# Kernel optimization log

Measured on AMD Instinct MI355X. Metric: run time of the kernel, lower is better.

## Reference

```python
import jax, jax.numpy as jnp
import numpy as np

N_NODES = 100000
N_EDGES = 1600000
DIM = 128
N_LAYERS = 3
BN_EPS = 1e-5


def setup_inputs() -> dict:
    key = jax.random.key(0)
    ks = jax.random.split(key, 8)
    x = jax.random.normal(ks[0], (N_NODES, DIM), dtype=jnp.float32)
    edge_index = jax.random.randint(ks[1], (2, N_EDGES), 0, N_NODES, dtype=jnp.int64)
    # Stacked per-layer params (all layers are DIM->DIM since input_dim==hidden_dim)
    W1 = jax.random.normal(ks[2], (N_LAYERS, DIM, DIM), dtype=jnp.float32) * 0.05
    b1 = jnp.zeros((N_LAYERS, DIM), dtype=jnp.float32)
    gamma = jnp.ones((N_LAYERS, DIM), dtype=jnp.float32)
    beta = jnp.zeros((N_LAYERS, DIM), dtype=jnp.float32)
    rmean = jnp.zeros((N_LAYERS, DIM), dtype=jnp.float32)
    rvar = jnp.ones((N_LAYERS, DIM), dtype=jnp.float32)
    W2 = jax.random.normal(ks[3], (N_LAYERS, DIM, DIM), dtype=jnp.float32) * 0.05
    b2 = jnp.zeros((N_LAYERS, DIM), dtype=jnp.float32)
    return {"x": x, "edge_index": edge_index, "W1": W1, "b1": b1,
            "gamma": gamma, "beta": beta, "rmean": rmean, "rvar": rvar,
            "W2": W2, "b2": b2}


def _gin_layer(h, src, dst, W1_l, b1_l, g_l, be_l, m_l, v_l, W2_l, b2_l):
    # adj_t @ h : sum of neighbor (src) features into dst nodes
    agg = jax.ops.segment_sum(h[src], dst, num_segments=N_NODES)
    h = h + agg  # (1 + eps) * x + agg, eps = 0
    h = h @ W1_l + b1_l
    # BatchNorm1d (inference mode, running stats)
    h = (h - m_l) * jax.lax.rsqrt(v_l + BN_EPS) * g_l + be_l
    h = jax.nn.relu(h)
    h = h @ W2_l + b2_l
    return jax.nn.relu(h)


def reference(x, edge_index, W1, b1, gamma, beta, rmean, rvar, W2, b2):
    src, dst = edge_index[0], edge_index[1]
    h = x
    for l in range(N_LAYERS):
        h = _gin_layer(h, src, dst, W1[l], b1[l], gamma[l], beta[l],
                       rmean[l], rvar[l], W2[l], b2[l])
        # dropout is identity in eval mode
    return jax.nn.log_softmax(h, axis=-1)
```

## Files before the change

### kernel.cpp

```cpp
#include <hip/hip_runtime.h>
#include <hip/hip_bf16.h>
#include <cstdint>

#define DIM 128
#define ASTR 136
#define WSTR 136
#define NBKT 512
#define BCAP 4608
#define NBIN_BLK 640

typedef __bf16 bf16x8 __attribute__((ext_vector_type(8)));
typedef float  f32x4  __attribute__((ext_vector_type(4)));
typedef unsigned short u16x8 __attribute__((ext_vector_type(8)));
typedef unsigned short u16x4 __attribute__((ext_vector_type(4)));

__device__ __forceinline__ unsigned short f2bf(float f) {
    union { float f; unsigned u; } x; x.f = f;
    unsigned r = x.u + 0x7fffu + ((x.u >> 16) & 1u);
    return (unsigned short)(r >> 16);
}
__device__ __forceinline__ float2 bfpair2f(unsigned v) {
    union { unsigned u; float f; } a, b;
    a.u = (v & 0xffffu) << 16;
    b.u = v & 0xffff0000u;
    return make_float2(a.f, b.f);
}

__global__ void detect_idx64(const unsigned* __restrict__ e, int* __restrict__ flag) {
    if (threadIdx.x == 0 && blockIdx.x == 0) {
        int is64 = 1;
        for (int i = 0; i < 32; ++i) {
            if (e[2 * i + 1] != 0u) { is64 = 0; break; }
        }
        *flag = is64;
    }
}

__device__ __forceinline__ void load_edge(const unsigned* __restrict__ eidx,
                                          int e, int E, int is64,
                                          int& s, int& d) {
    if (is64) {
        s = (int)eidx[2 * (size_t)e];
        d = (int)eidx[2 * ((size_t)E + (size_t)e)];
    } else {
        s = (int)eidx[(size_t)e];
        d = (int)eidx[(size_t)E + (size_t)e];
    }
}

__global__ __launch_bounds__(256) void prep_w(
    const float* __restrict__ W1, const float* __restrict__ W2,
    unsigned short* __restrict__ Wt)
{
    int id = blockIdx.x * 256 + threadIdx.x;
    if (id >= 3 * 2 * 16384) return;
    int l = id / 32768;
    int r = id - l * 32768;
    int w = r >> 14;
    int idx = r & 16383;
    int k = idx >> 7, n = idx & 127;
    const float* src = (w ? W2 : W1) + (size_t)l * 16384;
    Wt[(size_t)id - idx + ((size_t)n * 128 + k)] = f2bf(src[k * 128 + n]);
}

__global__ void prep_aff(const float* __restrict__ b1, const float* __restrict__ g,
                         const float* __restrict__ be, const float* __restrict__ m,
                         const float* __restrict__ v,
                         float* __restrict__ affA, float* __restrict__ affB)
{
    int id = blockIdx.x * 256 + threadIdx.x;
    if (id >= 3 * DIM) return;
    float A = g[id] * rsqrtf(v[id] + 1e-5f);
    affA[id] = A;
    affB[id] = (b1[id] - m[id]) * A + be[id];
}

__global__ __launch_bounds__(256) void x2bf(
    const float4* __restrict__ X, u16x4* __restrict__ O, int n4)
{
    int id = blockIdx.x * 256 + threadIdx.x;
    if (id >= n4) return;
    float4 v = X[id];
    u16x4 o;
    o[0] = f2bf(v.x); o[1] = f2bf(v.y); o[2] = f2bf(v.z); o[3] = f2bf(v.w);
    O[id] = o;
}

__global__ __launch_bounds__(256) void bin_edges(
    const unsigned* __restrict__ eidx, int E, const int* __restrict__ flag,
    int* __restrict__ gpos, unsigned* __restrict__ binned)
{
    __shared__ int cnt[NBKT];
    __shared__ int bas[NBKT];
    const int t = threadIdx.x;
    const int chunk = (E + gridDim.x - 1) / gridDim.x;
    const int e0 = blockIdx.x * chunk;
    const int e1 = (e0 + chunk < E) ? e0 + chunk : E;
    const int is64 = *flag;

    for (int b = t; b < NBKT; b += 256) cnt[b] = 0;
    __syncthreads();
    for (int e = e0 + t; e < e1; e += 256) {
        int s, d; load_edge(eidx, e, E, is64, s, d);
        atomicAdd(&cnt[d >> 8], 1);
    }
    __syncthreads();
    for (int b = t; b < NBKT; b += 256) {
        int c = cnt[b];
        bas[b] = c ? atomicAdd(&gpos[b], c) : 0;
    }
    __syncthreads();
    for (int e = e0 + t; e < e1; e += 256) {
        int s, d; load_edge(eidx, e, E, is64, s, d);
        int bk = d >> 8;
        int slot = atomicAdd(&bas[bk], 1);
        if (slot < BCAP)
            binned[(size_t)bk * BCAP + slot] = ((unsigned)s << 8) | (unsigned)(d & 255);
    }
}

__global__ __launch_bounds__(512) void bucket_scan(
    const int* __restrict__ gpos, int* __restrict__ bbase)
{
    __shared__ int sh[NBKT];
    int t = threadIdx.x;
    int v = gpos[t];
    sh[t] = v;
    __syncthreads();
    #pragma unroll
    for (int ofs = 1; ofs < NBKT; ofs <<= 1) {
        int add = (t >= ofs) ? sh[t - ofs] : 0;
        __syncthreads();
        sh[t] += add;
        __syncthreads();
    }
    bbase[t] = sh[t] - v;
}

__global__ __launch_bounds__(256) void bucket_fill(
    const unsigned* __restrict__ binned, const int* __restrict__ gpos,
    const int* __restrict__ bbase, int* __restrict__ off,
    int* __restrict__ csr, int M)
{
    __shared__ int cntL[256];
    __shared__ int sh[256];
    __shared__ int posL[256];
    const int b = blockIdx.x;
    const int t = threadIdx.x;
    int nb = gpos[b];
    nb = nb < BCAP ? nb : BCAP;
    const int base = bbase[b];

    cntL[t] = 0;
    __syncthreads();
    for (int i = t; i < nb; i += 256)
        atomicAdd(&cntL[binned[(size_t)b * BCAP + i] & 255], 1);
    __syncthreads();
    sh[t] = cntL[t];
    __syncthreads();
    #pragma unroll
    for (int ofs = 1; ofs < 256; ofs <<= 1) {
        int add = (t >= ofs) ? sh[t - ofs] : 0;
        __syncthreads();
        sh[t] += add;
        __syncthreads();
    }
    int excl = sh[t] - cntL[t];
    int node = b * 256 + t;
    if (node <= M) off[node] = base + excl;
    posL[t] = excl;
    __syncthreads();
    for (int i = t; i < nb; i += 256) {
        unsigned v = binned[(size_t)b * BCAP + i];
        int slot = atomicAdd(&posL[v & 255], 1);
        csr[base + slot] = (int)(v >> 8);
    }
}

__device__ __forceinline__ void acc_u4(float* acc, uint4 w) {
    float2 p;
    p = bfpair2f(w.x); acc[0] += p.x; acc[1] += p.y;
    p = bfpair2f(w.y); acc[2] += p.x; acc[3] += p.y;
    p = bfpair2f(w.z); acc[4] += p.x; acc[5] += p.y;
    p = bfpair2f(w.w); acc[6] += p.x; acc[7] += p.y;
}

__global__ __launch_bounds__(256) void gather_v(
    const uint4* __restrict__ Hv,
    const int* __restrict__ off, const int* __restrict__ csr,
    uint4* __restrict__ AGv, int M)
{
    int node = (blockIdx.x * 256 + threadIdx.x) >> 6;
    if (node >= M) return;
    int lane = threadIdx.x & 63;
    int q = lane >> 4, li = lane & 15;

    float acc[8] = {0.f, 0.f, 0.f, 0.f, 0.f, 0.f, 0.f, 0.f};
    if (q == 0) {
        uint4 w = Hv[(size_t)node * 16 + li];
        acc_u4(acc, w);
    }

    int beg = off[node], end = off[node + 1];
    int j = beg;
    for (; j + 16 <= end; j += 16) {
        int sA = csr[j + q];
        int sB = csr[j + 4 + q];
        int sC = csr[j + 8 + q];
        int sD = csr[j + 12 + q];
        uint4 wA = Hv[(size_t)sA * 16 + li];
        uint4 wB = Hv[(size_t)sB * 16 + li];
        uint4 wC = Hv[(size_t)sC * 16 + li];
        uint4 wD = Hv[(size_t)sD * 16 + li];
        acc_u4(acc, wA);
        acc_u4(acc, wB);
        acc_u4(acc, wC);
        acc_u4(acc, wD);
    }
    for (; j < end; j += 4) {
        int jj = j + q;
        int sx = csr[jj < end ? jj : end - 1];
        uint4 w = Hv[(size_t)sx * 16 + li];
        if (jj < end) acc_u4(acc, w);
    }

    #pragma unroll
    for (int k = 0; k < 8; ++k) {
        acc[k] += __shfl_xor(acc[k], 16);
        acc[k] += __shfl_xor(acc[k], 32);
    }
    if (q == 0) {
        uint4 o;
        o.x = (unsigned)f2bf(acc[0]) | ((unsigned)f2bf(acc[1]) << 16);
        o.y = (unsigned)f2bf(acc[2]) | ((unsigned)f2bf(acc[3]) << 16);
        o.z = (unsigned)f2bf(acc[4]) | ((unsigned)f2bf(acc[5]) << 16);
        o.w = (unsigned)f2bf(acc[6]) | ((unsigned)f2bf(acc[7]) << 16);
        AGv[(size_t)node * 16 + li] = o;
    }
}

template<int LAST>
__global__ __launch_bounds__(256) void fused_layer(
    const unsigned short* __restrict__ AGGb,
    const unsigned short* __restrict__ W1t,
    const unsigned short* __restrict__ W2t,
    const float* __restrict__ affA, const float* __restrict__ affB,
    const float* __restrict__ b2, void* __restrict__ OUTp, int M)
{
    __shared__ unsigned short Asub[64 * ASTR];
    __shared__ unsigned short Wsub[128 * WSTR];
    const int t = threadIdx.x;
    const int row0 = blockIdx.x * 64;
    const int w = t >> 6;
    const int lane = t & 63;
    const int lm = lane & 15;
    const int quad = lane >> 4;

    #pragma unroll
    for (int i = 0; i < 4; ++i) {
        int idx = t + 256 * i;
        int row = idx >> 4, ch = idx & 15;
        int gr = row0 + row;
        u16x8 v = {0, 0, 0, 0, 0, 0, 0, 0};
        if (gr < M) v = ((const u16x8*)(AGGb + (size_t)gr * DIM))[ch];
        *(u16x8*)&Asub[row * ASTR + ch * 8] = v;
    }
    #pragma unroll
    for (int i = 0; i < 16; ++i) {
        int idx = t + 256 * i;
        int n = idx >> 5, kc = idx & 31;
        *(ushort4*)&Wsub[n * WSTR + kc * 4] = ((const ushort4*)W1t)[idx];
    }
    __syncthreads();

    const int arow = w * 16 + lm;
    f32x4 acc[8];
    #pragma unroll
    for (int i = 0; i < 8; ++i) { f32x4 z = {0.f, 0.f, 0.f, 0.f}; acc[i] = z; }
    #pragma unroll
    for (int kc = 0; kc < 4; ++kc) {
        int k0 = kc * 32 + quad * 8;
        bf16x8 a = *(const bf16x8*)&Asub[arow * ASTR + k0];
        #pragma unroll
        for (int tt = 0; tt < 8; ++tt) {
            bf16x8 b = *(const bf16x8*)&Wsub[(tt * 16 + lm) * WSTR + k0];
            acc[tt] = __builtin_amdgcn_mfma_f32_16x16x32_bf16(a, b, acc[tt], 0, 0, 0);
        }
    }

    #pragma unroll
    for (int tt = 0; tt < 8; ++tt) {
        int c = tt * 16 + lm;
        float aA = affA[c], aB = affB[c];
        #pragma unroll
        for (int r = 0; r < 4; ++r) {
            float h = fmaxf(acc[tt][r] * aA + aB, 0.f);
            Asub[(w * 16 + quad * 4 + r) * ASTR + c] = f2bf(h);
        }
    }
    __syncthreads();
    #pragma unroll
    for (int i = 0; i < 16; ++i) {
        int idx = t + 256 * i;
        int n = idx >> 5, kc = idx & 31;
        *(ushort4*)&Wsub[n * WSTR + kc * 4] = ((const ushort4*)W2t)[idx];
    }
    __syncthreads();

    f32x4 acc2[8];
    #pragma unroll
    for (int i = 0; i < 8; ++i) { f32x4 z = {0.f, 0.f, 0.f, 0.f}; acc2[i] = z; }
    #pragma unroll
    for (int kc = 0; kc < 4; ++kc) {
        int k0 = kc * 32 + quad * 8;
        bf16x8 a = *(const bf16x8*)&Asub[arow * ASTR + k0];
        #pragma unroll
        for (int tt = 0; tt < 8; ++tt) {
            bf16x8 b = *(const bf16x8*)&Wsub[(tt * 16 + lm) * WSTR + k0];
            acc2[tt] = __builtin_amdgcn_mfma_f32_16x16x32_bf16(a, b, acc2[tt], 0, 0, 0);
        }
    }

    float v[8][4];
    #pragma unroll
    for (int tt = 0; tt < 8; ++tt) {
        int c = tt * 16 + lm;
        float bb = b2[c];
        #pragma unroll
        for (int r = 0; r < 4; ++r)
            v[tt][r] = fmaxf(acc2[tt][r] + bb, 0.f);
    }

    if (!LAST) {
        unsigned short* OUT = (unsigned short*)OUTp;
        #pragma unroll
        for (int tt = 0; tt < 8; ++tt) {
            int c = tt * 16 + lm;
            #pragma unroll
            for (int r = 0; r < 4; ++r) {
                int gr = row0 + w * 16 + quad * 4 + r;
                if (gr < M) OUT[(size_t)gr * DIM + c] = f2bf(v[tt][r]);
            }
        }
    } else {
        float* OUT = (float*)OUTp;
        #pragma unroll
        for (int r = 0; r < 4; ++r) {
            float mm = v[0][r];
            #pragma unroll
            for (int tt = 1; tt < 8; ++tt) mm = fmaxf(mm, v[tt][r]);
            #pragma unroll
            for (int ofs = 1; ofs < 16; ofs <<= 1)
                mm = fmaxf(mm, __shfl_xor(mm, ofs));
            float ss = 0.f;
            #pragma unroll
            for (int tt = 0; tt < 8; ++tt) ss += __expf(v[tt][r] - mm);
            #pragma unroll
            for (int ofs = 1; ofs < 16; ofs <<= 1)
                ss += __shfl_xor(ss, ofs);
            float lse = mm + __logf(ss);
            int gr = row0 + w * 16 + quad * 4 + r;
            if (gr < M) {
                #pragma unroll
                for (int tt = 0; tt < 8; ++tt)
                    OUT[(size_t)gr * DIM + tt * 16 + lm] = v[tt][r] - lse;
            }
        }
    }
}

static inline size_t align256(size_t v) { return (v + 255) & ~(size_t)255; }

extern "C" void kernel_launch(void* const* d_in, const int* in_sizes, int n_in,
                              void* d_out, int out_size, void* d_ws, size_t ws_size,
                              hipStream_t stream) {
    const float*    x     = (const float*)d_in[0];
    const unsigned* eidx  = (const unsigned*)d_in[1];
    const float*    W1    = (const float*)d_in[2];
    const float*    b1    = (const float*)d_in[3];
    const float*    gamma = (const float*)d_in[4];
    const float*    beta  = (const float*)d_in[5];
    const float*    rmean = (const float*)d_in[6];
    const float*    rvar  = (const float*)d_in[7];
    const float*    W2    = (const float*)d_in[8];
    const float*    b2    = (const float*)d_in[9];

    const int M = in_sizes[0] / DIM;
    const int E = in_sizes[1] / 2;
    const size_t hbf_bytes = (size_t)M * DIM * 2;

    float* out = (float*)d_out;
    char*  ws  = (char*)d_ws;

    size_t o = 0;
    int* flag = (int*)(ws + o);                     o = align256(o + 4);
    unsigned short* Wt = (unsigned short*)(ws + o); o = align256(o + (size_t)3 * 2 * 16384 * 2);
    float* affA = (float*)(ws + o);                 o = align256(o + 3 * DIM * 4);
    float* affB = (float*)(ws + o);                 o = align256(o + 3 * DIM * 4);
    int* gpos  = (int*)(ws + o);                    o = align256(o + NBKT * 4);
    int* bbase = (int*)(ws + o);                    o = align256(o + NBKT * 4);
    int* off   = (int*)(ws + o);                    o = align256(o + ((size_t)M + 1) * 4);
    int* csr   = (int*)(ws + o);                    o = align256(o + (size_t)E * 4);
    unsigned short* P = (unsigned short*)(ws + o);  o = align256(o + hbf_bytes);
    unsigned short* Q = (unsigned short*)(ws + o);  o = align256(o + hbf_bytes);
    unsigned* binned = (unsigned*)Q;

    detect_idx64<<<1, 64, 0, stream>>>(eidx, flag);
    prep_w<<<(3 * 2 * 16384 + 255) / 256, 256, 0, stream>>>(W1, W2, Wt);
    prep_aff<<<2, 256, 0, stream>>>(b1, gamma, beta, rmean, rvar, affA, affB);
    x2bf<<<(M * 32 + 255) / 256, 256, 0, stream>>>(
        (const float4*)x, (u16x4*)P, M * 32);

    hipMemsetAsync(gpos, 0, NBKT * 4, stream);
    bin_edges<<<NBIN_BLK, 256, 0, stream>>>(eidx, E, flag, gpos, binned);
    bucket_scan<<<1, 512, 0, stream>>>(gpos, bbase);
    bucket_fill<<<NBKT, 256, 0, stream>>>(binned, gpos, bbase, off, csr, M);

    const int gat_blocks  = (M + 3) / 4;
    const int fuse_blocks = (M + 63) / 64;

    gather_v<<<gat_blocks, 256, 0, stream>>>((const uint4*)P, off, csr,
                                             (uint4*)Q, M);
    fused_layer<0><<<fuse_blocks, 256, 0, stream>>>(
        Q, Wt + 0 * 16384, Wt + 1 * 16384,
        affA + 0 * DIM, affB + 0 * DIM, b2 + 0 * DIM, (void*)P, M);
    gather_v<<<gat_blocks, 256, 0, stream>>>((const uint4*)P, off, csr,
                                             (uint4*)Q, M);
    fused_layer<0><<<fuse_blocks, 256, 0, stream>>>(
        Q, Wt + 2 * 16384, Wt + 3 * 16384,
        affA + 1 * DIM, affB + 1 * DIM, b2 + 1 * DIM, (void*)P, M);
    gather_v<<<gat_blocks, 256, 0, stream>>>((const uint4*)P, off, csr,
                                             (uint4*)Q, M);
    fused_layer<1><<<fuse_blocks, 256, 0, stream>>>(
        Q, Wt + 4 * 16384, Wt + 5 * 16384,
        affA + 2 * DIM, affB + 2 * DIM, b2 + 2 * DIM, (void*)out, M);
}
```

Before: 445.0 us.

## Merge prep kernels, stage edges in LDS for binning, fold scan, deepen gather unroll

Combines the index-width detection, weight transpose, affine precompute, x-to-bf16 conversion and gpos zeroing into a single launch, replacing a memset and several small kernels. The edge binner now buffers packed edges in shared memory so edge indices are read from global memory once instead of twice, using more blocks with fixed chunks. The bucket prefix scan is recomputed redundantly inside every bucket_fill block, removing one launch. The gather loop issues eight neighbour loads per batch with masked tails to raise memory-level parallelism, at the cost of extra registers and some wasted loads on short rows.

```diff
diff --git a/kernel.cpp b/kernel.cpp
--- a/kernel.cpp
+++ b/kernel.cpp
@@ -7,7 +7,7 @@
 #define WSTR 136
 #define NBKT 512
 #define BCAP 4608
-#define NBIN_BLK 640
+#define ECHUNK 2500
 
 typedef __bf16 bf16x8 __attribute__((ext_vector_type(8)));
 typedef float  f32x4  __attribute__((ext_vector_type(4)));
@@ -21,19 +21,9 @@
 }
 __device__ __forceinline__ float2 bfpair2f(unsigned v) {
     union { unsigned u; float f; } a, b;
-    a.u = (v & 0xffffu) << 16;
+    a.u = v << 16;
     b.u = v & 0xffff0000u;
     return make_float2(a.f, b.f);
-}
-
-__global__ void detect_idx64(const unsigned* __restrict__ e, int* __restrict__ flag) {
-    if (threadIdx.x == 0 && blockIdx.x == 0) {
-        int is64 = 1;
-        for (int i = 0; i < 32; ++i) {
-            if (e[2 * i + 1] != 0u) { is64 = 0; break; }
-        }
-        *flag = is64;
-    }
 }
 
 __device__ __forceinline__ void load_edge(const unsigned* __restrict__ eidx,
@@ -48,42 +38,50 @@
     }
 }
 
-__global__ __launch_bounds__(256) void prep_w(
+__global__ __launch_bounds__(256) void prep_all(
+    const float* __restrict__ x,
     const float* __restrict__ W1, const float* __restrict__ W2,
-    unsigned short* __restrict__ Wt)
+    const float* __restrict__ b1, const float* __restrict__ g,
+    const float* __restrict__ be, const float* __restrict__ m,
+    const float* __restrict__ v, const unsigned* __restrict__ eidx,
+    unsigned short* __restrict__ Wt, float* __restrict__ affA,
+    float* __restrict__ affB, u16x4* __restrict__ P,
+    int* __restrict__ flag, int* __restrict__ gpos,
+    int M, int xblk, int wblk)
 {
-    int id = blockIdx.x * 256 + threadIdx.x;
-    if (id >= 3 * 2 * 16384) return;
-    int l = id / 32768;
-    int r = id - l * 32768;
-    int w = r >> 14;
-    int idx = r & 16383;
-    int k = idx >> 7, n = idx & 127;
-    const float* src = (w ? W2 : W1) + (size_t)l * 16384;
-    Wt[(size_t)id - idx + ((size_t)n * 128 + k)] = f2bf(src[k * 128 + n]);
-}
-
-__global__ void prep_aff(const float* __restrict__ b1, const float* __restrict__ g,
-                         const float* __restrict__ be, const float* __restrict__ m,
-                         const float* __restrict__ v,
-                         float* __restrict__ affA, float* __restrict__ affB)
-{
-    int id = blockIdx.x * 256 + threadIdx.x;
-    if (id >= 3 * DIM) return;
-    float A = g[id] * rsqrtf(v[id] + 1e-5f);
-    affA[id] = A;
-    affB[id] = (b1[id] - m[id]) * A + be[id];
-}
-
-__global__ __launch_bounds__(256) void x2bf(
-    const float4* __restrict__ X, u16x4* __restrict__ O, int n4)
-{
-    int id = blockIdx.x * 256 + threadIdx.x;
-    if (id >= n4) return;
-    float4 v = X[id];
-    u16x4 o;
-    o[0] = f2bf(v.x); o[1] = f2bf(v.y); o[2] = f2bf(v.z); o[3] = f2bf(v.w);
-    O[id] = o;
+    const int b = blockIdx.x, t = threadIdx.x;
+    if (b < xblk) {
+        int id = b * 256 + t;
+        if (id < M * 32) {
+            float4 vv = ((const float4*)x)[id];
+            u16x4 o;
+            o[0] = f2bf(vv.x); o[1] = f2bf(vv.y);
+            o[2] = f2bf(vv.z); o[3] = f2bf(vv.w);
+            P[id] = o;
+        }
+    } else if (b < xblk + wblk) {
+        int id = (b - xblk) * 256 + t;
+        int l = id / 32768;
+        int r = id - l * 32768;
+        int w = r >> 14;
+        int idx = r & 16383;
+        int k = idx >> 7, n = idx & 127;
+        const float* src = (w ? W2 : W1) + (size_t)l * 16384;
+        Wt[(size_t)id - idx + ((size_t)n * 128 + k)] = f2bf(src[k * 128 + n]);
+    } else {
+        for (int id = t; id < 3 * DIM; id += 256) {
+            float A = g[id] * rsqrtf(v[id] + 1e-5f);
+            affA[id] = A;
+            affB[id] = (b1[id] - m[id]) * A + be[id];
+        }
+        for (int id = t; id < NBKT; id += 256) gpos[id] = 0;
+        if (t == 0) {
+            int is64 = 1;
+            for (int i = 0; i < 32; ++i)
+                if (eidx[2 * i + 1] != 0u) { is64 = 0; break; }
+            *flag = is64;
+        }
+    }
 }
 
 __global__ __launch_bounds__(256) void bin_edges(
@@ -92,64 +90,59 @@
 {
     __shared__ int cnt[NBKT];
     __shared__ int bas[NBKT];
+    __shared__ unsigned pk[ECHUNK];
+    __shared__ unsigned short bkL[ECHUNK];
     const int t = threadIdx.x;
-    const int chunk = (E + gridDim.x - 1) / gridDim.x;
-    const int e0 = blockIdx.x * chunk;
-    const int e1 = (e0 + chunk < E) ? e0 + chunk : E;
+    const int e0 = blockIdx.x * ECHUNK;
+    int n = E - e0; if (n > ECHUNK) n = ECHUNK;
     const int is64 = *flag;
 
-    for (int b = t; b < NBKT; b += 256) cnt[b] = 0;
-    __syncthreads();
-    for (int e = e0 + t; e < e1; e += 256) {
-        int s, d; load_edge(eidx, e, E, is64, s, d);
-        atomicAdd(&cnt[d >> 8], 1);
-    }
-    __syncthreads();
-    for (int b = t; b < NBKT; b += 256) {
-        int c = cnt[b];
-        bas[b] = c ? atomicAdd(&gpos[b], c) : 0;
-    }
-    __syncthreads();
-    for (int e = e0 + t; e < e1; e += 256) {
-        int s, d; load_edge(eidx, e, E, is64, s, d);
+    for (int i = t; i < NBKT; i += 256) cnt[i] = 0;
+    __syncthreads();
+    for (int i = t; i < n; i += 256) {
+        int s, d; load_edge(eidx, e0 + i, E, is64, s, d);
         int bk = d >> 8;
+        pk[i] = ((unsigned)s << 8) | (unsigned)(d & 255);
+        bkL[i] = (unsigned short)bk;
+        atomicAdd(&cnt[bk], 1);
+    }
+    __syncthreads();
+    for (int i = t; i < NBKT; i += 256) {
+        int c = cnt[i];
+        bas[i] = c ? atomicAdd(&gpos[i], c) : 0;
+    }
+    __syncthreads();
+    for (int i = t; i < n; i += 256) {
+        int bk = bkL[i];
         int slot = atomicAdd(&bas[bk], 1);
         if (slot < BCAP)
-            binned[(size_t)bk * BCAP + slot] = ((unsigned)s << 8) | (unsigned)(d & 255);
-    }
-}
-
-__global__ __launch_bounds__(512) void bucket_scan(
-    const int* __restrict__ gpos, int* __restrict__ bbase)
-{
-    __shared__ int sh[NBKT];
-    int t = threadIdx.x;
-    int v = gpos[t];
-    sh[t] = v;
-    __syncthreads();
-    #pragma unroll
-    for (int ofs = 1; ofs < NBKT; ofs <<= 1) {
-        int add = (t >= ofs) ? sh[t - ofs] : 0;
-        __syncthreads();
-        sh[t] += add;
-        __syncthreads();
-    }
-    bbase[t] = sh[t] - v;
+            binned[(size_t)bk * BCAP + slot] = pk[i];
+    }
 }
 
 __global__ __launch_bounds__(256) void bucket_fill(
     const unsigned* __restrict__ binned, const int* __restrict__ gpos,
-    const int* __restrict__ bbase, int* __restrict__ off,
-    int* __restrict__ csr, int M)
+    int* __restrict__ off, int* __restrict__ csr, int M)
 {
+    __shared__ int sc[NBKT];
     __shared__ int cntL[256];
     __shared__ int sh[256];
     __shared__ int posL[256];
     const int b = blockIdx.x;
     const int t = threadIdx.x;
-    int nb = gpos[b];
-    nb = nb < BCAP ? nb : BCAP;
-    const int base = bbase[b];
+
+    sc[t]       = min(gpos[t], BCAP);
+    sc[t + 256] = min(gpos[t + 256], BCAP);
+    __syncthreads();
+    for (int ofs = 1; ofs < NBKT; ofs <<= 1) {
+        int a0 = (t >= ofs) ? sc[t - ofs] : 0;
+        int a1 = sc[t + 256 - ofs];
+        __syncthreads();
+        sc[t] += a0; sc[t + 256] += a1;
+        __syncthreads();
+    }
+    const int nb   = min(gpos[b], BCAP);
+    const int base = sc[b] - nb;
 
     cntL[t] = 0;
     __syncthreads();
@@ -171,18 +164,15 @@
     posL[t] = excl;
     __syncthreads();
     for (int i = t; i < nb; i += 256) {
-        unsigned v = binned[(size_t)b * BCAP + i];
-        int slot = atomicAdd(&posL[v & 255], 1);
-        csr[base + slot] = (int)(v >> 8);
-    }
-}
-
-__device__ __forceinline__ void acc_u4(float* acc, uint4 w) {
-    float2 p;
-    p = bfpair2f(w.x); acc[0] += p.x; acc[1] += p.y;
-    p = bfpair2f(w.y); acc[2] += p.x; acc[3] += p.y;
-    p = bfpair2f(w.z); acc[4] += p.x; acc[5] += p.y;
-    p = bfpair2f(w.w); acc[6] += p.x; acc[7] += p.y;
+        unsigned vv = binned[(size_t)b * BCAP + i];
+        int slot = atomicAdd(&posL[vv & 255], 1);
+        csr[base + slot] = (int)(vv >> 8);
+    }
+}
+
+__device__ __forceinline__ void addpair(float2& a, unsigned v) {
+    float2 p = bfpair2f(v);
+    a.x += p.x; a.y += p.y;
 }
 
 __global__ __launch_bounds__(256) void gather_v(
@@ -195,46 +185,48 @@
     int lane = threadIdx.x & 63;
     int q = lane >> 4, li = lane & 15;
 
-    float acc[8] = {0.f, 0.f, 0.f, 0.f, 0.f, 0.f, 0.f, 0.f};
+    float2 acc[4];
+    acc[0] = acc[1] = acc[2] = acc[3] = make_float2(0.f, 0.f);
     if (q == 0) {
         uint4 w = Hv[(size_t)node * 16 + li];
-        acc_u4(acc, w);
-    }
-
-    int beg = off[node], end = off[node + 1];
-    int j = beg;
-    for (; j + 16 <= end; j += 16) {
-        int sA = csr[j + q];
-        int sB = csr[j + 4 + q];
-        int sC = csr[j + 8 + q];
-        int sD = csr[j + 12 + q];
-        uint4 wA = Hv[(size_t)sA * 16 + li];
-        uint4 wB = Hv[(size_t)sB * 16 + li];
-        uint4 wC = Hv[(size_t)sC * 16 + li];
-        uint4 wD = Hv[(size_t)sD * 16 + li];
-        acc_u4(acc, wA);
-        acc_u4(acc, wB);
-        acc_u4(acc, wC);
-        acc_u4(acc, wD);
-    }
-    for (; j < end; j += 4) {
-        int jj = j + q;
-        int sx = csr[jj < end ? jj : end - 1];
-        uint4 w = Hv[(size_t)sx * 16 + li];
-        if (jj < end) acc_u4(acc, w);
-    }
-
-    #pragma unroll
-    for (int k = 0; k < 8; ++k) {
-        acc[k] += __shfl_xor(acc[k], 16);
-        acc[k] += __shfl_xor(acc[k], 32);
+        acc[0] = bfpair2f(w.x); acc[1] = bfpair2f(w.y);
+        acc[2] = bfpair2f(w.z); acc[3] = bfpair2f(w.w);
+    }
+
+    const int beg = off[node], end = off[node + 1];
+    for (int jb = beg; jb < end; jb += 32) {
+        int idx[8];
+        uint4 w[8];
+        #pragma unroll
+        for (int u = 0; u < 8; ++u) {
+            idx[u] = jb + u * 4 + q;
+            int ic = idx[u] < end ? idx[u] : end - 1;
+            int s = csr[ic];
+            w[u] = Hv[(size_t)s * 16 + li];
+        }
+        #pragma unroll
+        for (int u = 0; u < 8; ++u) {
+            if (idx[u] >= end) { w[u].x = 0; w[u].y = 0; w[u].z = 0; w[u].w = 0; }
+            addpair(acc[0], w[u].x);
+            addpair(acc[1], w[u].y);
+            addpair(acc[2], w[u].z);
+            addpair(acc[3], w[u].w);
+        }
+    }
+
+    #pragma unroll
+    for (int k = 0; k < 4; ++k) {
+        acc[k].x += __shfl_xor(acc[k].x, 16);
+        acc[k].y += __shfl_xor(acc[k].y, 16);
+        acc[k].x += __shfl_xor(acc[k].x, 32);
+        acc[k].y += __shfl_xor(acc[k].y, 32);
     }
     if (q == 0) {
         uint4 o;
-        o.x = (unsigned)f2bf(acc[0]) | ((unsigned)f2bf(acc[1]) << 16);
-        o.y = (unsigned)f2bf(acc[2]) | ((unsigned)f2bf(acc[3]) << 16);
-        o.z = (unsigned)f2bf(acc[4]) | ((unsigned)f2bf(acc[5]) << 16);
-        o.w = (unsigned)f2bf(acc[6]) | ((unsigned)f2bf(acc[7]) << 16);
+        o.x = (unsigned)f2bf(acc[0].x) | ((unsigned)f2bf(acc[0].y) << 16);
+        o.y = (unsigned)f2bf(acc[1].x) | ((unsigned)f2bf(acc[1].y) << 16);
+        o.z = (unsigned)f2bf(acc[2].x) | ((unsigned)f2bf(acc[2].y) << 16);
+        o.w = (unsigned)f2bf(acc[3].x) | ((unsigned)f2bf(acc[3].y) << 16);
         AGv[(size_t)node * 16 + li] = o;
     }
 }
@@ -398,23 +390,21 @@
     float* affA = (float*)(ws + o);                 o = align256(o + 3 * DIM * 4);
     float* affB = (float*)(ws + o);                 o = align256(o + 3 * DIM * 4);
     int* gpos  = (int*)(ws + o);                    o = align256(o + NBKT * 4);
-    int* bbase = (int*)(ws + o);                    o = align256(o + NBKT * 4);
     int* off   = (int*)(ws + o);                    o = align256(o + ((size_t)M + 1) * 4);
     int* csr   = (int*)(ws + o);                    o = align256(o + (size_t)E * 4);
     unsigned short* P = (unsigned short*)(ws + o);  o = align256(o + hbf_bytes);
     unsigned short* Q = (unsigned short*)(ws + o);  o = align256(o + hbf_bytes);
     unsigned* binned = (unsigned*)Q;
 
-    detect_idx64<<<1, 64, 0, stream>>>(eidx, flag);
-    prep_w<<<(3 * 2 * 16384 + 255) / 256, 256, 0, stream>>>(W1, W2, Wt);
-    prep_aff<<<2, 256, 0, stream>>>(b1, gamma, beta, rmean, rvar, affA, affB);
-    x2bf<<<(M * 32 + 255) / 256, 256, 0, stream>>>(
-        (const float4*)x, (u16x4*)P, M * 32);
-
-    hipMemsetAsync(gpos, 0, NBKT * 4, stream);
-    bin_edges<<<NBIN_BLK, 256, 0, stream>>>(eidx, E, flag, gpos, binned);
-    bucket_scan<<<1, 512, 0, stream>>>(gpos, bbase);
-    bucket_fill<<<NBKT, 256, 0, stream>>>(binned, gpos, bbase, off, csr, M);
+    const int xblk = (M * 32 + 255) / 256;
+    const int wblk = (3 * 2 * 16384 + 255) / 256;
+    prep_all<<<xblk + wblk + 1, 256, 0, stream>>>(
+        x, W1, W2, b1, gamma, beta, rmean, rvar, eidx,
+        Wt, affA, affB, (u16x4*)P, flag, gpos, M, xblk, wblk);
+
+    const int bblk = (E + ECHUNK - 1) / ECHUNK;
+    bin_edges<<<bblk, 256, 0, stream>>>(eidx, E, flag, gpos, binned);
+    bucket_fill<<<NBKT, 256, 0, stream>>>(binned, gpos, off, csr, M);
 
     const int gat_blocks  = (M + 3) / 4;
     const int fuse_blocks = (M + 63) / 64;
```

Measured after the change: 419.6 us. -5.7%, faster.
